# Optimization experiments

Measured on AMD Instinct MI355X. Metric: run time of the kernel, lower is better.

The kernel has to match this reference:

```python
import jax, jax.numpy as jnp
import numpy as np

N_POS = 10  # number of child positions encoded in U_f (10*h_size rows)


def setup_inputs() -> dict:
    key = jax.random.key(0)
    ks = jax.random.split(key, 12)
    N, H = 32768, 128
    s = 0.05  # keep activations in a sane range
    return {
        "child_h": jax.random.normal(ks[0], (N, 1, H), jnp.float32),
        "child_c": jax.random.normal(ks[1], (N, 1, H), jnp.float32),
        "extra_input_depth_1": jax.random.normal(ks[2], (N, H), jnp.float32),
        "extra_input_depth_2": jax.random.normal(ks[3], (N, H), jnp.float32),
        "h_prev": jax.random.normal(ks[4], (N, H), jnp.float32),
        "pos": jax.random.randint(ks[5], (N,), 0, N_POS, jnp.int32),
        "depth": jax.random.randint(ks[6], (N,), 0, 4, jnp.int32),
        "mask": jax.random.randint(ks[7], (N,), 0, 2, jnp.int32),
        "W_f": jax.random.normal(ks[8], (N_POS * H, H), jnp.float32) * s,
        "b_f": jax.random.normal(ks[9], (N_POS * H,), jnp.float32) * s,
        "W_iou": jax.random.normal(ks[10], (3 * H, N_POS * H), jnp.float32) * s,
        "b_iou": jax.random.normal(ks[11], (1, 3 * H), jnp.float32) * s,
    }


def reference(child_h, child_c, extra_input_depth_1, extra_input_depth_2,
              h_prev, pos, depth, mask, W_f, b_f, W_iou, b_iou):
    N, _, H = child_h.shape
    dt = child_h.dtype
    # reduce_func: flatten mailbox (single child => last_dim == h_size)
    h_cat = child_h.reshape(N, H)
    # masked injection of extra inputs by depth
    h_cat = h_cat + extra_input_depth_2 * (depth == 2).astype(dt)[:, None]
    h_cat = h_cat + extra_input_depth_1 * (depth == 1).astype(dt)[:, None]
    # per-position grouped matmuls against weight slices, scattered back by pos mask
    W_f_r = W_f.reshape(N_POS, H, H)          # row slice pos*H:(pos+1)*H
    b_f_r = b_f.reshape(N_POS, H)
    W_iou_r = W_iou.reshape(3 * H, N_POS, H)  # col slice pos*H:(pos+1)*H
    u = jnp.zeros((N, H), dt)
    iou = jnp.zeros((N, 3 * H), dt)
    for p in range(N_POS):  # small fixed group count
        sel = (pos == p)[:, None]
        u = jnp.where(sel, h_cat @ W_f_r[p] + b_f_r[p][None, :], u)
        iou = jnp.where(sel, h_cat @ W_iou_r[:, p, :].T, iou)
    # sigmoid forget gate, children-sum of cell states
    f = jax.nn.sigmoid(u)
    c_red = jnp.sum(f[:, None, :] * child_c, axis=1)  # [N, H]
    # apply_node_func
    iou = iou + b_iou
    i, o, uu = jnp.split(iou, 3, axis=1)
    c_new = jax.nn.sigmoid(i) * jnp.tanh(uu) + c_red
    h_new = jax.nn.sigmoid(o) * jnp.tanh(c_new)
    # update_masked_nodes=False: blend (note: DGL node 'c' was overwritten by reduce)
    m = mask.astype(dt)[:, None]
    h = h_prev * m + (1.0 - m) * h_new
    c = c_red * m + (1.0 - m) * c_new
    return h, c
```

## Files before the change

kernel.cpp:

```cpp
#include <hip/hip_runtime.h>

#define H 128
#define NPOS 10
#define ROWSB 32
#define BLOCK 512

using bf16x8 = __attribute__((ext_vector_type(8))) short;
using f32x4  = __attribute__((ext_vector_type(4))) float;

__device__ __forceinline__ unsigned short f2bf(float f) {
  unsigned u = __float_as_uint(f);
  u += 0x7FFFu + ((u >> 16) & 1u);
  return (unsigned short)(u >> 16);
}
__device__ __forceinline__ float sigm(float x) {
  return __builtin_amdgcn_rcpf(1.0f + __builtin_amdgcn_exp2f(-1.44269504f * x));
}
__device__ __forceinline__ float tanh_f(float x) {
  return 2.0f * __builtin_amdgcn_rcpf(1.0f + __builtin_amdgcn_exp2f(-2.88539008f * x)) - 1.0f;
}

__global__ void prep_wt(const float* __restrict__ Wf, const float* __restrict__ Wiou,
                        unsigned short* __restrict__ wt,
                        const int* __restrict__ posp, int* __restrict__ hist2,
                        int N, int nhb) {
  int b = blockIdx.x, t = threadIdx.x;
  if (b < NPOS * 16) {
    __shared__ float tile[32][33];
    int p = b >> 4, jt = (b >> 2) & 3, kt = b & 3;
    int tx = t & 31, ty = t >> 5;
    #pragma unroll
    for (int it = 0; it < 4; ++it) {
      int krow = kt * 32 + ty + it * 8;
      int j = jt * 32 + tx;
      tile[ty + it * 8][tx] = Wf[(size_t)(p * H + krow) * H + j];
    }
    __syncthreads();
    #pragma unroll
    for (int it = 0; it < 4; ++it) {
      int j2 = jt * 32 + ty + it * 8;
      int k2 = kt * 32 + tx;
      size_t dst = (((size_t)(p * 4 + kt) * 4 + (tx >> 3)) * 512 + j2) * 8 + (tx & 7);
      wt[dst] = f2bf(tile[tx][ty + it * 8]);
    }
  } else if (b < NPOS * 16 + (NPOS * 384 * H) / 256) {
    int id = (b - NPOS * 16) * 256 + t;
    int p = id / 49152;
    int r = id - p * 49152;
    int j = 128 + (r >> 7);
    int k = r & 127;
    float v = Wiou[(size_t)(r >> 7) * (NPOS * H) + p * H + k];
    size_t dst = (((size_t)(p * 4 + (k >> 5)) * 4 + ((k >> 3) & 3)) * 512 + j) * 8 + (k & 7);
    wt[dst] = f2bf(v);
  } else {
    int hb = b - (NPOS * 16 + (NPOS * 384 * H) / 256);
    __shared__ int c[NPOS];
    if (t < NPOS) c[t] = 0;
    __syncthreads();
    int i = hb * 256 + t;
    if (i < N) atomicAdd(&c[posp[i]], 1);
    __syncthreads();
    if (t < NPOS) hist2[hb * 16 + t] = c[t];
  }
}

__global__ void scan_build(const int* __restrict__ hist2, int nhb,
                           int* __restrict__ off2,
                           int* __restrict__ blkpos, int* __restrict__ blkgs,
                           int* __restrict__ blkcnt, int maxb) {
  __shared__ int tot[NPOS], base[NPOS + 1], bb[NPOS + 1];
  int t = threadIdx.x;
  int w = t >> 6, l = t & 63;
  if (w < NPOS) {
    int b0 = 2 * l, b1 = 2 * l + 1;
    int a  = (b0 < nhb) ? hist2[b0 * 16 + w] : 0;
    int bv = (b1 < nhb) ? hist2[b1 * 16 + w] : 0;
    int s = a + bv, sc = s;
    #pragma unroll
    for (int off = 1; off < 64; off <<= 1) {
      int u = __shfl_up(sc, off);
      if (l >= off) sc += u;
    }
    int excl = sc - s;
    if (b0 < nhb) off2[b0 * 16 + w] = excl;
    if (b1 < nhb) off2[b1 * 16 + w] = excl + a;
    if (l == 63) tot[w] = sc;
  }
  __syncthreads();
  if (t == 0) {
    int run = 0, rb = 0;
    for (int p = 0; p < NPOS; ++p) {
      base[p] = run; bb[p] = rb;
      run += tot[p];
      rb += (tot[p] + ROWSB - 1) / ROWSB;
    }
    base[NPOS] = run; bb[NPOS] = rb;
  }
  __syncthreads();
  for (int i = t; i < nhb * NPOS; i += 640) {
    int b = i / NPOS, p = i - b * NPOS;
    off2[b * 16 + p] += base[p];
  }
  int nb = bb[NPOS];
  for (int b = t; b < maxb; b += 640) {
    if (b < nb) {
      int p = 0;
      while (bb[p + 1] <= b) ++p;
      int s = (b - bb[p]) * ROWSB;
      blkpos[b] = p;
      blkgs[b] = base[p] + s;
      blkcnt[b] = min(ROWSB, tot[p] - s);
    } else {
      blkpos[b] = -1;
    }
  }
}

__global__ void scatter_idx(const int* __restrict__ posp, const int* __restrict__ depthp,
                            const int* __restrict__ maskp, const int* __restrict__ off2,
                            unsigned* __restrict__ order, int N) {
  __shared__ int c[NPOS], basearr[NPOS];
  int hb = blockIdx.x, t = threadIdx.x;
  if (t < NPOS) { c[t] = 0; basearr[t] = off2[hb * 16 + t]; }
  __syncthreads();
  int i = hb * 256 + t;
  int p = -1, r = 0;
  unsigned e = 0;
  if (i < N) {
    p = posp[i];
    r = atomicAdd(&c[p], 1);
    int d = depthp[i];
    int mk = maskp[i];
    e = (unsigned)i | ((unsigned)mk << 16) |
        ((unsigned)(d == 1) << 17) | ((unsigned)(d == 2) << 18);
  }
  __syncthreads();
  if (p >= 0) order[basearr[p] + r] = e;
}

__global__ __launch_bounds__(BLOCK, 3) void tree_lstm_main(
    const float* __restrict__ child_h, const float* __restrict__ child_c,
    const float* __restrict__ e1, const float* __restrict__ e2,
    const float* __restrict__ h_prev,
    const float* __restrict__ b_f, const float* __restrict__ b_iou,
    const unsigned short* __restrict__ wt,
    const unsigned* __restrict__ order, const int* __restrict__ blkpos,
    const int* __restrict__ blkgs, const int* __restrict__ blkcnt,
    float* __restrict__ out, int N) {

  const int b = blockIdx.x;
  const int p = blkpos[b];
  if (p < 0) return;
  const int gs = blkgs[b], cnth = blkcnt[b];

  __shared__ unsigned short hs[ROWSB * H];
  __shared__ unsigned short Bs[4 * 512 * 8];
  __shared__ unsigned rowg[ROWSB];

  const int t = threadIdx.x;
  const int wv = t >> 6, l = t & 63;
  const int l15 = l & 15, lhi = l >> 4;
  const int colr = wv * 16 + l15;

  if (t < ROWSB) rowg[t] = (t < cnth) ? order[gs + t] : 0xFFFFFFFFu;
  __syncthreads();

  {
    int row = t >> 4, c8 = t & 15;
    unsigned e = rowg[row];
    float4 a0 = {0.f, 0.f, 0.f, 0.f}, a1 = {0.f, 0.f, 0.f, 0.f};
    if ((int)e >= 0) {
      int g = e & 0xFFFF;
      const float4* ph = (const float4*)(child_h + (size_t)g * H + c8 * 8);
      a0 = ph[0]; a1 = ph[1];
      if (e & (3u << 17)) {
        const float* ep = (e & (1u << 17)) ? e1 : e2;
        const float4* pe = (const float4*)(ep + (size_t)g * H + c8 * 8);
        float4 b0 = pe[0], b1 = pe[1];
        a0.x += b0.x; a0.y += b0.y; a0.z += b0.z; a0.w += b0.w;
        a1.x += b1.x; a1.y += b1.y; a1.z += b1.z; a1.w += b1.w;
      }
    }
    bf16x8 v;
    v[0] = (short)f2bf(a0.x); v[1] = (short)f2bf(a0.y);
    v[2] = (short)f2bf(a0.z); v[3] = (short)f2bf(a0.w);
    v[4] = (short)f2bf(a1.x); v[5] = (short)f2bf(a1.y);
    v[6] = (short)f2bf(a1.z); v[7] = (short)f2bf(a1.w);
    int wb = (row * 256 + c8 * 16) ^ ((row & 7) << 4);
    *(bf16x8*)((char*)hs + wb) = v;
  }

  unsigned gg[2][4]; float cc[2][4], hpv[2][4];
  #pragma unroll
  for (int c = 0; c < 2; ++c)
    #pragma unroll
    for (int q = 0; q < 4; ++q) {
      int rr = c * 16 + lhi * 4 + q;
      unsigned e = (rr < cnth) ? rowg[rr] : 0xFFFFFFFFu;
      gg[c][q] = e;
      if ((int)e >= 0) {
        size_t gi = (size_t)(e & 0xFFFF) * H + colr;
        cc[c][q] = child_c[gi];
        hpv[c][q] = h_prev[gi];
      } else { cc[c][q] = 0.f; hpv[c][q] = 0.f; }
    }

  __syncthreads();

  f32x4 acc[2][4] = {};
  const unsigned short* wtp = wt + (size_t)p * 65536;

  #pragma unroll
  for (int kk = 0; kk < 4; ++kk) {
    if (kk) __syncthreads();
    #pragma unroll
    for (int i = 0; i < 4; ++i) {
      int eo = (i * BLOCK + t) * 8;
      *(bf16x8*)(Bs + eo) = *(const bf16x8*)(wtp + kk * 16384 + eo);
    }
    __syncthreads();

    bf16x8 bfr[4];
    #pragma unroll
    for (int g4 = 0; g4 < 4; ++g4)
      bfr[g4] = *(const bf16x8*)(Bs + ((lhi * 512) + (g4 * 128 + colr)) * 8);

    #pragma unroll
    for (int c = 0; c < 2; ++c) {
      const int arow = c * 16 + l15;
      int rb = (arow * 256 + kk * 64 + lhi * 16) ^ ((arow & 7) << 4);
      bf16x8 afr = *(const bf16x8*)((const char*)hs + rb);
      #pragma unroll
      for (int g4 = 0; g4 < 4; ++g4)
        acc[c][g4] = __builtin_amdgcn_mfma_f32_16x16x32_bf16(afr, bfr[g4], acc[c][g4], 0, 0, 0);
    }
  }

  const size_t NH = (size_t)N * H;
  const float bfv = b_f[p * H + colr];
  const float b_i = b_iou[colr], b_o = b_iou[H + colr], b_g = b_iou[2 * H + colr];

  #pragma unroll
  for (int c = 0; c < 2; ++c)
    #pragma unroll
    for (int q = 0; q < 4; ++q) {
      if ((int)gg[c][q] >= 0) {
        size_t gi = (size_t)(gg[c][q] & 0xFFFF) * H + colr;
        float u  = acc[c][0][q] + bfv;
        float iv = acc[c][1][q] + b_i;
        float ov = acc[c][2][q] + b_o;
        float gv = acc[c][3][q] + b_g;
        float f = sigm(u);
        float credv = f * cc[c][q];
        float cnew = sigm(iv) * tanh_f(gv) + credv;
        float hnew = sigm(ov) * tanh_f(cnew);
        float m = (float)((gg[c][q] >> 16) & 1u);
        float hv = hpv[c][q] * m + (1.0f - m) * hnew;
        float cv = credv * m + (1.0f - m) * cnew;
        out[gi] = hv;
        out[NH + gi] = cv;
      }
    }
}

extern "C" void kernel_launch(void* const* d_in, const int* in_sizes, int n_in,
                              void* d_out, int out_size, void* d_ws, size_t ws_size,
                              hipStream_t stream) {
  const float* child_h = (const float*)d_in[0];
  const float* child_c = (const float*)d_in[1];
  const float* e1      = (const float*)d_in[2];
  const float* e2      = (const float*)d_in[3];
  const float* h_prev  = (const float*)d_in[4];
  const int*   posp    = (const int*)d_in[5];
  const int*   depthp  = (const int*)d_in[6];
  const int*   maskp   = (const int*)d_in[7];
  const float* W_f     = (const float*)d_in[8];
  const float* b_f     = (const float*)d_in[9];
  const float* W_iou   = (const float*)d_in[10];
  const float* b_iou   = (const float*)d_in[11];
  float* out = (float*)d_out;
  int N = in_sizes[0] / H;
  int nhb = (N + 255) / 256;
  int maxb = NPOS + N / ROWSB;

  unsigned short* wt = (unsigned short*)d_ws;
  int* hist2  = (int*)((char*)d_ws + (size_t)NPOS * 512 * H * 2);
  int* off2   = hist2 + nhb * 16;
  int* blkpos = off2 + nhb * 16;
  int* blkgs  = blkpos + maxb;
  int* blkcnt = blkgs + maxb;
  unsigned* order = (unsigned*)(blkcnt + maxb);

  int prep_blocks = NPOS * 16 + (NPOS * 384 * H) / 256 + nhb;
  hipLaunchKernelGGL(prep_wt, dim3(prep_blocks), dim3(256), 0, stream,
                     W_f, W_iou, wt, posp, hist2, N, nhb);
  hipLaunchKernelGGL(scan_build, dim3(1), dim3(640), 0, stream,
                     hist2, nhb, off2, blkpos, blkgs, blkcnt, maxb);
  hipLaunchKernelGGL(scatter_idx, dim3(nhb), dim3(256), 0, stream,
                     posp, depthp, maskp, off2, order, N);
  hipLaunchKernelGGL(tree_lstm_main, dim3(maxb), dim3(BLOCK), 0, stream,
                     child_h, child_c, e1, e2, h_prev,
                     b_f, b_iou, wt, order, blkpos, blkgs, blkcnt, out, N);
}
```

Before: 47.24 us.

## Double the rows per block and prefetch weight slices into registers

Each block now handles 64 rows instead of 32, so every weight slice staged in shared memory is reused across twice as many rows. The next K-slice of weights is loaded into registers while the current slice's MFMAs run, then written to shared memory between barriers. The child_c and h_prev loads are deferred to the last K iteration so they overlap compute. The changes also use raw s_barrier with manual lgkmcnt waits instead of __syncthreads. The cost is higher register pressure from larger accumulator and prefetch arrays, fewer blocks (possibly more padded rows per position group), and reliance on hand-written barrier semantics for correctness.

```diff
diff --git a/kernel.cpp b/kernel.cpp
--- a/kernel.cpp
+++ b/kernel.cpp
@@ -2,7 +2,7 @@
 
 #define H 128
 #define NPOS 10
-#define ROWSB 32
+#define ROWSB 64
 #define BLOCK 512
 
 using bf16x8 = __attribute__((ext_vector_type(8))) short;
@@ -39,7 +39,6 @@
     #pragma unroll
     for (int it = 0; it < 4; ++it) {
       int j2 = jt * 32 + ty + it * 8;
-      int k2 = kt * 32 + tx;
       size_t dst = (((size_t)(p * 4 + kt) * 4 + (tx >> 3)) * 512 + j2) * 8 + (tx & 7);
       wt[dst] = f2bf(tile[tx][ty + it * 8]);
     }
@@ -163,10 +162,14 @@
   const int colr = wv * 16 + l15;
 
   if (t < ROWSB) rowg[t] = (t < cnth) ? order[gs + t] : 0xFFFFFFFFu;
-  __syncthreads();
-
-  {
-    int row = t >> 4, c8 = t & 15;
+  asm volatile("s_waitcnt lgkmcnt(0)");
+  __builtin_amdgcn_sched_barrier(0);
+  __builtin_amdgcn_s_barrier();
+
+  #pragma unroll
+  for (int i = 0; i < 2; ++i) {
+    int id = i * BLOCK + t;
+    int row = id >> 4, c8 = id & 15;
     unsigned e = rowg[row];
     float4 a0 = {0.f, 0.f, 0.f, 0.f}, a1 = {0.f, 0.f, 0.f, 0.f};
     if ((int)e >= 0) {
@@ -190,35 +193,45 @@
     *(bf16x8*)((char*)hs + wb) = v;
   }
 
-  unsigned gg[2][4]; float cc[2][4], hpv[2][4];
-  #pragma unroll
-  for (int c = 0; c < 2; ++c)
-    #pragma unroll
-    for (int q = 0; q < 4; ++q) {
-      int rr = c * 16 + lhi * 4 + q;
-      unsigned e = (rr < cnth) ? rowg[rr] : 0xFFFFFFFFu;
-      gg[c][q] = e;
-      if ((int)e >= 0) {
-        size_t gi = (size_t)(e & 0xFFFF) * H + colr;
-        cc[c][q] = child_c[gi];
-        hpv[c][q] = h_prev[gi];
-      } else { cc[c][q] = 0.f; hpv[c][q] = 0.f; }
-    }
-
-  __syncthreads();
-
-  f32x4 acc[2][4] = {};
   const unsigned short* wtp = wt + (size_t)p * 65536;
+  {
+    bf16x8 breg[4];
+    #pragma unroll
+    for (int i = 0; i < 4; ++i)
+      breg[i] = *(const bf16x8*)(wtp + (i * BLOCK + t) * 8);
+    #pragma unroll
+    for (int i = 0; i < 4; ++i)
+      *(bf16x8*)(Bs + (i * BLOCK + t) * 8) = breg[i];
+  }
+  asm volatile("s_waitcnt lgkmcnt(0)");
+  __builtin_amdgcn_sched_barrier(0);
+  __builtin_amdgcn_s_barrier();
+
+  f32x4 acc[4][4] = {};
+  unsigned gg[4][4]; float cc[4][4], hpv[4][4];
 
   #pragma unroll
   for (int kk = 0; kk < 4; ++kk) {
-    if (kk) __syncthreads();
-    #pragma unroll
-    for (int i = 0; i < 4; ++i) {
-      int eo = (i * BLOCK + t) * 8;
-      *(bf16x8*)(Bs + eo) = *(const bf16x8*)(wtp + kk * 16384 + eo);
-    }
-    __syncthreads();
+    bf16x8 nreg[4];
+    if (kk < 3) {
+      #pragma unroll
+      for (int i = 0; i < 4; ++i)
+        nreg[i] = *(const bf16x8*)(wtp + (kk + 1) * 16384 + (i * BLOCK + t) * 8);
+    } else {
+      #pragma unroll
+      for (int c = 0; c < 4; ++c)
+        #pragma unroll
+        for (int q = 0; q < 4; ++q) {
+          int rr = c * 16 + lhi * 4 + q;
+          unsigned e = (rr < cnth) ? rowg[rr] : 0xFFFFFFFFu;
+          gg[c][q] = e;
+          if ((int)e >= 0) {
+            size_t gi = (size_t)(e & 0xFFFF) * H + colr;
+            cc[c][q] = child_c[gi];
+            hpv[c][q] = h_prev[gi];
+          } else { cc[c][q] = 0.f; hpv[c][q] = 0.f; }
+        }
+    }
 
     bf16x8 bfr[4];
     #pragma unroll
@@ -226,7 +239,7 @@
       bfr[g4] = *(const bf16x8*)(Bs + ((lhi * 512) + (g4 * 128 + colr)) * 8);
 
     #pragma unroll
-    for (int c = 0; c < 2; ++c) {
+    for (int c = 0; c < 4; ++c) {
       const int arow = c * 16 + l15;
       int rb = (arow * 256 + kk * 64 + lhi * 16) ^ ((arow & 7) << 4);
       bf16x8 afr = *(const bf16x8*)((const char*)hs + rb);
@@ -234,6 +247,18 @@
       for (int g4 = 0; g4 < 4; ++g4)
         acc[c][g4] = __builtin_amdgcn_mfma_f32_16x16x32_bf16(afr, bfr[g4], acc[c][g4], 0, 0, 0);
     }
+
+    if (kk < 3) {
+      asm volatile("s_waitcnt lgkmcnt(0)");
+      __builtin_amdgcn_sched_barrier(0);
+      __builtin_amdgcn_s_barrier();
+      #pragma unroll
+      for (int i = 0; i < 4; ++i)
+        *(bf16x8*)(Bs + (i * BLOCK + t) * 8) = nreg[i];
+      asm volatile("s_waitcnt lgkmcnt(0)");
+      __builtin_amdgcn_sched_barrier(0);
+      __builtin_amdgcn_s_barrier();
+    }
   }
 
   const size_t NH = (size_t)N * H;
@@ -241,7 +266,7 @@
   const float b_i = b_iou[colr], b_o = b_iou[H + colr], b_g = b_iou[2 * H + colr];
 
   #pragma unroll
-  for (int c = 0; c < 2; ++c)
+  for (int c = 0; c < 4; ++c)
     #pragma unroll
     for (int q = 0; q < 4; ++q) {
       if ((int)gg[c][q] >= 0) {
```

Result: slower. 52.00 us (+10.1%).

## Stage gate pre-activations in LDS and run the epilogue row-major with coalesced accesses

Applied to the files above, without the earlier changes.

The MFMA accumulators plus biases are written to shared memory as bf16, then re-read so each wave handles whole rows with two adjacent columns per lane. This turns the scattered per-element child_c/h_prev loads and output stores into contiguous float2 accesses, skips the h_prev load and the gate math for masked rows, and uses nontemporal stores. The prefetch of child_c and h_prev before the matmul is removed, so those loads are no longer overlapped with compute. Rounding the gate values to bf16 adds precision loss, and the change adds two extra barriers.

```diff
diff --git a/kernel.cpp b/kernel.cpp
--- a/kernel.cpp
+++ b/kernel.cpp
@@ -12,6 +12,9 @@
   unsigned u = __float_as_uint(f);
   u += 0x7FFFu + ((u >> 16) & 1u);
   return (unsigned short)(u >> 16);
+}
+__device__ __forceinline__ float bf2f(unsigned short s) {
+  return __uint_as_float(((unsigned)s) << 16);
 }
 __device__ __forceinline__ float sigm(float x) {
   return __builtin_amdgcn_rcpf(1.0f + __builtin_amdgcn_exp2f(-1.44269504f * x));
@@ -39,7 +42,6 @@
     #pragma unroll
     for (int it = 0; it < 4; ++it) {
       int j2 = jt * 32 + ty + it * 8;
-      int k2 = kt * 32 + tx;
       size_t dst = (((size_t)(p * 4 + kt) * 4 + (tx >> 3)) * 512 + j2) * 8 + (tx & 7);
       wt[dst] = f2bf(tile[tx][ty + it * 8]);
     }
@@ -189,22 +191,6 @@
     int wb = (row * 256 + c8 * 16) ^ ((row & 7) << 4);
     *(bf16x8*)((char*)hs + wb) = v;
   }
-
-  unsigned gg[2][4]; float cc[2][4], hpv[2][4];
-  #pragma unroll
-  for (int c = 0; c < 2; ++c)
-    #pragma unroll
-    for (int q = 0; q < 4; ++q) {
-      int rr = c * 16 + lhi * 4 + q;
-      unsigned e = (rr < cnth) ? rowg[rr] : 0xFFFFFFFFu;
-      gg[c][q] = e;
-      if ((int)e >= 0) {
-        size_t gi = (size_t)(e & 0xFFFF) * H + colr;
-        cc[c][q] = child_c[gi];
-        hpv[c][q] = h_prev[gi];
-      } else { cc[c][q] = 0.f; hpv[c][q] = 0.f; }
-    }
-
   __syncthreads();
 
   f32x4 acc[2][4] = {};
@@ -235,32 +221,64 @@
         acc[c][g4] = __builtin_amdgcn_mfma_f32_16x16x32_bf16(afr, bfr[g4], acc[c][g4], 0, 0, 0);
     }
   }
+  __syncthreads();
+
+  {
+    const float bfv = b_f[p * H + colr];
+    const float b_i = b_iou[colr], b_o = b_iou[H + colr], b_g = b_iou[2 * H + colr];
+    #pragma unroll
+    for (int c = 0; c < 2; ++c)
+      #pragma unroll
+      for (int q = 0; q < 4; ++q) {
+        int r = c * 16 + lhi * 4 + q;
+        Bs[((r * 4 + 0) << 7) + colr] = f2bf(acc[c][0][q] + bfv);
+        Bs[((r * 4 + 1) << 7) + colr] = f2bf(acc[c][1][q] + b_i);
+        Bs[((r * 4 + 2) << 7) + colr] = f2bf(acc[c][2][q] + b_o);
+        Bs[((r * 4 + 3) << 7) + colr] = f2bf(acc[c][3][q] + b_g);
+      }
+  }
+  __syncthreads();
 
   const size_t NH = (size_t)N * H;
-  const float bfv = b_f[p * H + colr];
-  const float b_i = b_iou[colr], b_o = b_iou[H + colr], b_g = b_iou[2 * H + colr];
-
+  const int c2 = 2 * l;
   #pragma unroll
-  for (int c = 0; c < 2; ++c)
-    #pragma unroll
-    for (int q = 0; q < 4; ++q) {
-      if ((int)gg[c][q] >= 0) {
-        size_t gi = (size_t)(gg[c][q] & 0xFFFF) * H + colr;
-        float u  = acc[c][0][q] + bfv;
-        float iv = acc[c][1][q] + b_i;
-        float ov = acc[c][2][q] + b_o;
-        float gv = acc[c][3][q] + b_g;
-        float f = sigm(u);
-        float credv = f * cc[c][q];
-        float cnew = sigm(iv) * tanh_f(gv) + credv;
-        float hnew = sigm(ov) * tanh_f(cnew);
-        float m = (float)((gg[c][q] >> 16) & 1u);
-        float hv = hpv[c][q] * m + (1.0f - m) * hnew;
-        float cv = credv * m + (1.0f - m) * cnew;
-        out[gi] = hv;
-        out[NH + gi] = cv;
+  for (int j = 0; j < 4; ++j) {
+    int r = wv * 4 + j;
+    unsigned e = rowg[r];
+    if ((int)e >= 0) {
+      int g = e & 0xFFFF;
+      int mi = (e >> 16) & 1;
+      unsigned uw = *(const unsigned*)&Bs[((r * 4 + 0) << 7) + c2];
+      unsigned iw = *(const unsigned*)&Bs[((r * 4 + 1) << 7) + c2];
+      unsigned ow = *(const unsigned*)&Bs[((r * 4 + 2) << 7) + c2];
+      unsigned gw = *(const unsigned*)&Bs[((r * 4 + 3) << 7) + c2];
+      float2 ccv = *(const float2*)(child_c + (size_t)g * H + c2);
+      float f0 = sigm(bf2f((unsigned short)(uw & 0xFFFF)));
+      float f1 = sigm(bf2f((unsigned short)(uw >> 16)));
+      float cr0 = f0 * ccv.x, cr1 = f1 * ccv.y;
+      float h0, h1, cv0, cv1;
+      if (mi) {
+        float2 hp = *(const float2*)(h_prev + (size_t)g * H + c2);
+        h0 = hp.x; h1 = hp.y; cv0 = cr0; cv1 = cr1;
+      } else {
+        float i0 = sigm(bf2f((unsigned short)(iw & 0xFFFF)));
+        float i1 = sigm(bf2f((unsigned short)(iw >> 16)));
+        float g0 = tanh_f(bf2f((unsigned short)(gw & 0xFFFF)));
+        float g1 = tanh_f(bf2f((unsigned short)(gw >> 16)));
+        float o0 = sigm(bf2f((unsigned short)(ow & 0xFFFF)));
+        float o1 = sigm(bf2f((unsigned short)(ow >> 16)));
+        cv0 = i0 * g0 + cr0;
+        cv1 = i1 * g1 + cr1;
+        h0 = o0 * tanh_f(cv0);
+        h1 = o1 * tanh_f(cv1);
       }
-    }
+      size_t gi = (size_t)g * H + c2;
+      __builtin_nontemporal_store(h0, &out[gi]);
+      __builtin_nontemporal_store(h1, &out[gi + 1]);
+      __builtin_nontemporal_store(cv0, &out[NH + gi]);
+      __builtin_nontemporal_store(cv1, &out[NH + gi + 1]);
+    }
+  }
 }
 
 extern "C" void kernel_launch(void* const* d_in, const int* in_sizes, int n_in,
```

Measured after the change: 44.89 us. 5.0% less time.
